# Kernel tuning notes

Measured on AMD Instinct MI355X. Metric: run time of the kernel, lower is better.

Reference implementation:

```python
import jax, jax.numpy as jnp
import numpy as np

E = 8        # num discriminators == num adapters (layer_structure = [1]*8)
D = 1024     # feature_dim
DO = 1024    # out_feature_dim
R = 64       # adapter bottleneck rank
H = 256      # discriminator hidden dim
B, T = 8, 2048


def setup_inputs() -> dict:
    key = jax.random.key(0)
    ks = jax.random.split(key, 12)
    s = lambda k, shape, fan: jax.random.normal(k, shape, jnp.float32) / np.sqrt(fan)
    return {
        "x": jax.random.normal(ks[0], (B, T, D), jnp.float32),
        # base layer (Linear D -> DO)
        "W_base": s(ks[1], (D, DO), D),
        "b_base": jnp.zeros((DO,), jnp.float32),
        # stacked discriminator autoencoders: D -> H -> D
        "Wd1": s(ks[2], (E, D, H), D),
        "bd1": jnp.zeros((E, H), jnp.float32),
        "Wd2": s(ks[3], (E, H, D), H),
        "bd2": jnp.zeros((E, D), jnp.float32),
        # stacked bottleneck adapters: D -> R -> DO
        "Wa_down": s(ks[4], (E, D, R), D),
        "ba_down": jnp.zeros((E, R), jnp.float32),
        "Wa_up": s(ks[5], (E, R, DO), R),
        "ba_up": jnp.zeros((E, DO), jnp.float32),
    }


def reference(x, W_base, b_base, Wd1, bd1, Wd2, bd2, Wa_down, ba_down, Wa_up, ba_up):
    # base path
    base = jnp.einsum("btd,do->bto", x, W_base) + b_base

    # all discriminators in parallel (stack_module_state + vmap equivalent)
    h = jax.nn.relu(jnp.einsum("btd,edh->ebth", x, Wd1) + bd1[:, None, None, :])
    recon = jnp.einsum("ebth,ehd->ebtd", h, Wd2) + bd2[:, None, None, :]
    # per-(discriminator, sample) reconstruction loss -> [E, B]
    losses = jnp.mean((recon - x[None]) ** 2, axis=(2, 3))

    # top-1 routing: argmin over discriminators per sample; identity mapping to adapters
    idx = jnp.argmin(losses, axis=0)  # [B]

    # grouped adapter forward: gather per-sample weights, batched GEMM
    a = jax.nn.relu(jnp.einsum("btd,bdr->btr", x, Wa_down[idx]) + ba_down[idx][:, None, :])
    adapter_out = jnp.einsum("btr,bro->bto", a, Wa_up[idx]) + ba_up[idx][:, None, :]

    return base + adapter_out
```

## Files before the change

kernel.cpp:

```cpp
#include <hip/hip_runtime.h>

typedef __bf16 bf16x8 __attribute__((ext_vector_type(8)));
typedef float f32x4 __attribute__((ext_vector_type(4)));
typedef unsigned short ushort_t;

#define THREADS 256
#define PTHREADS 512

__device__ __forceinline__ unsigned short f2bf(float f) {
  unsigned int u = __builtin_bit_cast(unsigned int, f);
  u += 0x7fffu + ((u >> 16) & 1u);
  return (unsigned short)(u >> 16);
}

__device__ __forceinline__ float bf2f(ushort_t u) {
  unsigned int v = ((unsigned int)u) << 16;
  return __builtin_bit_cast(float, v);
}

__device__ __forceinline__ void gload_lds16(const ushort_t* g, ushort_t* l) {
  __builtin_amdgcn_global_load_lds(
      (const __attribute__((address_space(1))) void*)g,
      (__attribute__((address_space(3))) void*)l, 16, 0, 0);
}

template <int N>
__device__ __forceinline__ void wait_vmcnt() {
  if constexpr (N == 0)
    asm volatile("s_waitcnt vmcnt(0)" ::: "memory");
  else if constexpr (N == 3)
    asm volatile("s_waitcnt vmcnt(3)" ::: "memory");
  else if constexpr (N == 6)
    asm volatile("s_waitcnt vmcnt(6)" ::: "memory");
}

__device__ __forceinline__ void block_barrier() {
  asm volatile("" ::: "memory");
  __builtin_amdgcn_s_barrier();
  asm volatile("" ::: "memory");
}

__device__ __forceinline__ int argmin8(const float* __restrict__ losses,
                                       int sample) {
  float best = losses[sample];
  int bi = 0;
#pragma unroll
  for (int e = 1; e < 8; ++e) {
    float v = losses[e * 8 + sample];
    if (v < best) { best = v; bi = e; }
  }
  return bi;
}

__global__ void transpose_all_kernel(
    const float* __restrict__ Wd1, const float* __restrict__ Wd2,
    const float* __restrict__ Wb, const float* __restrict__ Wad,
    const float* __restrict__ Wau, const float4* __restrict__ x4,
    ushort_t* __restrict__ Wd1T, ushort_t* __restrict__ Wd2T,
    ushort_t* __restrict__ WbT, ushort_t* __restrict__ WadT,
    ushort_t* __restrict__ WauT, ushort4* __restrict__ x_bf4,
    float* __restrict__ losses) {
  __shared__ float t[32][33];
  int b = blockIdx.x;
  int tx = threadIdx.x, ty = threadIdx.y;
  int ft = ty * 32 + tx;
  if (b == 0 && ft < 64) losses[ft] = 0.f;

  if (b >= 6144) {
    int base = (b - 6144) * 2048 + ft;
#pragma unroll
    for (int i = 0; i < 8; ++i) {
      float4 v = x4[base + i * 256];
      ushort4 o;
      o.x = f2bf(v.x); o.y = f2bf(v.y); o.z = f2bf(v.z); o.w = f2bf(v.w);
      x_bf4[base + i * 256] = o;
    }
    return;
  }

  const float* src;
  ushort_t* dst;
  int R, C, z, cx, ry;
  if (b < 2048) {
    src = Wd1; dst = Wd1T; R = 1024; C = 256;
    z = b >> 8; int rem = b & 255; cx = rem & 7; ry = rem >> 3;
  } else if (b < 4096) {
    int bb = b - 2048;
    src = Wd2; dst = Wd2T; R = 256; C = 1024;
    z = bb >> 8; int rem = bb & 255; cx = rem & 31; ry = rem >> 5;
  } else if (b < 5120) {
    int bb = b - 4096;
    src = Wb; dst = WbT; R = 1024; C = 1024;
    z = 0; cx = bb & 31; ry = bb >> 5;
  } else if (b < 5632) {
    int bb = b - 5120;
    src = Wad; dst = WadT; R = 1024; C = 64;
    z = bb >> 6; int rem = bb & 63; cx = rem & 1; ry = rem >> 1;
  } else {
    int bb = b - 5632;
    src = Wau; dst = WauT; R = 64; C = 1024;
    z = bb >> 6; int rem = bb & 63; cx = rem & 31; ry = rem >> 5;
  }
  size_t zoff = (size_t)z * R * C;
  src += zoff; dst += zoff;
  int c0 = cx * 32, r0 = ry * 32;
#pragma unroll
  for (int i = 0; i < 4; ++i)
    t[ty + 8 * i][tx] = src[(size_t)(r0 + ty + 8 * i) * C + c0 + tx];
  __syncthreads();
#pragma unroll
  for (int i = 0; i < 4; ++i)
    dst[(size_t)(c0 + ty + 8 * i) * R + r0 + tx] = f2bf(t[tx][ty + 8 * i]);
}

#define ACC_ZERO(acc, MM, NN)                        \
  _Pragma("unroll") for (int _i = 0; _i < MM; ++_i)  \
  _Pragma("unroll") for (int _j = 0; _j < NN; ++_j)  \
      acc[_i][_j] = (f32x4){0.f, 0.f, 0.f, 0.f};

__device__ __forceinline__ int sw(int row) { return (row >> 1) & 3; }

__device__ __forceinline__ bf16x8 frag_sw(const ushort_t* lds, int row, int q) {
  int slot = q ^ sw(row);
  return *(const bf16x8*)(lds + (row * 4 + slot) * 8);
}

template <int BM, int BN, int NT>
__device__ __forceinline__ void stage_p(const ushort_t* __restrict__ A,
                                        size_t lda, int arow0,
                                        const ushort_t* __restrict__ BT,
                                        size_t ldb, int brow0, int k0,
                                        ushort_t* As, ushort_t* Bs, int tid) {
#pragma unroll
  for (int i = 0; i < BM * 4 / NT; ++i) {
    int c = tid + i * NT;
    int row = c >> 2, slot = c & 3;
    int g = slot ^ sw(row);
    gload_lds16(A + (size_t)(arow0 + row) * lda + k0 + g * 8, As + c * 8);
  }
#pragma unroll
  for (int i = 0; i < BN * 4 / NT; ++i) {
    int c = tid + i * NT;
    int row = c >> 2, slot = c & 3;
    int g = slot ^ sw(row);
    gload_lds16(BT + (size_t)(brow0 + row) * ldb + k0 + g * 8, Bs + c * 8);
  }
}

#define PIPE_LDS_BYTES ((3 * (256 * 32) + 3 * (128 * 32)) * 2)

template <int BM, int BN>
__device__ __forceinline__ void pipe_kloop84(const ushort_t* __restrict__ A,
                                             size_t lda, int arow0,
                                             const ushort_t* __restrict__ BT,
                                             size_t ldb, int brow0, int K,
                                             ushort_t* smem, int tid, int wm,
                                             int wn, f32x4 acc[8][4]) {
  constexpr int ASLOT = BM * 32, BSLOT = BN * 32;
  ushort_t* Asl = smem;
  ushort_t* Bsl = smem + 3 * ASLOT;
  int lane = tid & 63;
  int r = lane & 15, q = lane >> 4;
  int nt = K >> 5;
  stage_p<BM, BN, THREADS>(A, lda, arow0, BT, ldb, brow0, 0, Asl, Bsl, tid);
  if (nt > 1)
    stage_p<BM, BN, THREADS>(A, lda, arow0, BT, ldb, brow0, 32, Asl + ASLOT,
                             Bsl + BSLOT, tid);
  for (int t = 0; t < nt; ++t) {
    if (t + 1 < nt)
      wait_vmcnt<6>();
    else
      wait_vmcnt<0>();
    block_barrier();
    if (t + 2 < nt) {
      int s = (t + 2) % 3;
      stage_p<BM, BN, THREADS>(A, lda, arow0, BT, ldb, brow0, (t + 2) * 32,
                               Asl + s * ASLOT, Bsl + s * BSLOT, tid);
    }
    int cur = t % 3;
    const ushort_t* Ac = Asl + cur * ASLOT;
    const ushort_t* Bc = Bsl + cur * BSLOT;
    bf16x8 af[8], bg[4];
#pragma unroll
    for (int mi = 0; mi < 8; ++mi)
      af[mi] = frag_sw(Ac, wm * 128 + mi * 16 + r, q);
#pragma unroll
    for (int ni = 0; ni < 4; ++ni)
      bg[ni] = frag_sw(Bc, wn * 64 + ni * 16 + r, q);
    __builtin_amdgcn_s_setprio(1);
#pragma unroll
    for (int mi = 0; mi < 8; ++mi)
#pragma unroll
      for (int ni = 0; ni < 4; ++ni)
        acc[mi][ni] = __builtin_amdgcn_mfma_f32_16x16x32_bf16(
            af[mi], bg[ni], acc[mi][ni], 0, 0, 0);
    __builtin_amdgcn_s_setprio(0);
  }
  block_barrier();
}

template <int BM, int BN>
__device__ __forceinline__ void pipe_kloop44(const ushort_t* __restrict__ A,
                                             size_t lda, int arow0,
                                             const ushort_t* __restrict__ BT,
                                             size_t ldb, int brow0, int K,
                                             ushort_t* smem, int tid, int wm,
                                             int wn, f32x4 acc[4][4]) {
  constexpr int ASLOT = BM * 32, BSLOT = BN * 32;
  ushort_t* Asl = smem;
  ushort_t* Bsl = smem + 3 * ASLOT;
  int lane = tid & 63;
  int r = lane & 15, q = lane >> 4;
  int nt = K >> 5;
  stage_p<BM, BN, PTHREADS>(A, lda, arow0, BT, ldb, brow0, 0, Asl, Bsl, tid);
  if (nt > 1)
    stage_p<BM, BN, PTHREADS>(A, lda, arow0, BT, ldb, brow0, 32, Asl + ASLOT,
                              Bsl + BSLOT, tid);
  for (int t = 0; t < nt; ++t) {
    if (t + 1 < nt)
      wait_vmcnt<3>();
    else
      wait_vmcnt<0>();
    block_barrier();
    if (t + 2 < nt) {
      int s = (t + 2) % 3;
      stage_p<BM, BN, PTHREADS>(A, lda, arow0, BT, ldb, brow0, (t + 2) * 32,
                                Asl + s * ASLOT, Bsl + s * BSLOT, tid);
    }
    int cur = t % 3;
    const ushort_t* Ac = Asl + cur * ASLOT;
    const ushort_t* Bc = Bsl + cur * BSLOT;
    bf16x8 af[4], bg[4];
#pragma unroll
    for (int mi = 0; mi < 4; ++mi)
      af[mi] = frag_sw(Ac, wm * 64 + mi * 16 + r, q);
#pragma unroll
    for (int ni = 0; ni < 4; ++ni)
      bg[ni] = frag_sw(Bc, wn * 64 + ni * 16 + r, q);
    __builtin_amdgcn_s_setprio(1);
#pragma unroll
    for (int mi = 0; mi < 4; ++mi)
#pragma unroll
      for (int ni = 0; ni < 4; ++ni)
        acc[mi][ni] = __builtin_amdgcn_mfma_f32_16x16x32_bf16(
            af[mi], bg[ni], acc[mi][ni], 0, 0, 0);
    __builtin_amdgcn_s_setprio(0);
  }
  block_barrier();
}

__global__ __launch_bounds__(THREADS, 2) void disc_h_kernel(
    const ushort_t* __restrict__ x_bf, const ushort_t* __restrict__ Wd1T,
    const float* __restrict__ bd1, ushort_t* __restrict__ h) {
  extern __shared__ ushort_t smem[];
  int b = blockIdx.x;
  int work = (b & 7) * 128 + (b >> 3);
  int m0 = (work >> 4) * 256;
  int n0 = (work & 15) * 128;
  int tid = threadIdx.x, wid = tid >> 6, lane = tid & 63;
  int wm = wid >> 1, wn = wid & 1;
  f32x4 acc[8][4];
  ACC_ZERO(acc, 8, 4);
  pipe_kloop84<256, 128>(x_bf, 1024, m0, Wd1T, 1024, n0, 1024, smem, tid, wm,
                         wn, acc);
  int r = lane & 15, q = lane >> 4;
#pragma unroll
  for (int ni = 0; ni < 4; ++ni) {
    int col = n0 + wn * 64 + ni * 16 + r;
    float bias = bd1[col];
    int e = col >> 8, nn = col & 255;
    ushort_t* hp = h + (size_t)e * 16384 * 256 + nn;
#pragma unroll
    for (int mi = 0; mi < 8; ++mi) {
      int rowb = m0 + wm * 128 + mi * 16 + q * 4;
#pragma unroll
      for (int j = 0; j < 4; ++j) {
        float v = fmaxf(acc[mi][ni][j] + bias, 0.f);
        hp[(size_t)(rowb + j) * 256] = f2bf(v);
      }
    }
  }
}

__global__ __launch_bounds__(PTHREADS, 4) void disc_loss_kernel(
    const ushort_t* __restrict__ h, const ushort_t* __restrict__ Wd2T,
    const float* __restrict__ bd2, const ushort_t* __restrict__ x_bf,
    float* __restrict__ losses) {
  extern __shared__ ushort_t smem[];
  __shared__ float red[8];
  int b = blockIdx.x;
  int work = (b & 7) * 512 + (b >> 3);
  int e = work >> 9;
  int m0 = ((work >> 3) & 63) * 256;
  int n0 = (work & 7) * 128;
  int tid = threadIdx.x, wid = tid >> 6, lane = tid & 63;
  int wm = wid >> 1, wn = wid & 1;
  int r = lane & 15, q = lane >> 4;
  const ushort_t* hA = h + (size_t)e * 16384 * 256;
  const ushort_t* W2 = Wd2T + (size_t)e * 1024 * 256;

  f32x4 acc[4][4];
  ACC_ZERO(acc, 4, 4);
  pipe_kloop44<256, 128>(hA, 256, m0, W2, 256, n0, 256, smem, tid, wm, wn,
                         acc);

  float s = 0.f;
#pragma unroll
  for (int ni = 0; ni < 4; ++ni) {
    int colg = n0 + wn * 64 + ni * 16 + r;
    float bias = bd2[e * 1024 + colg];
#pragma unroll
    for (int mi = 0; mi < 4; ++mi) {
      int rowg = m0 + wm * 64 + mi * 16 + q * 4;
#pragma unroll
      for (int j = 0; j < 4; ++j) {
        float v = acc[mi][ni][j] + bias -
                  bf2f(x_bf[(size_t)(rowg + j) * 1024 + colg]);
        s += v * v;
      }
    }
  }
#pragma unroll
  for (int off = 32; off > 0; off >>= 1) s += __shfl_down(s, off);
  if (lane == 0) red[wid] = s;
  __syncthreads();
  if (tid == 0) {
    float t = 0.f;
#pragma unroll
    for (int i = 0; i < 8; ++i) t += red[i];
    atomicAdd(&losses[e * 8 + (m0 >> 11)], t);
  }
}

__global__ __launch_bounds__(THREADS, 2) void final_kernel(
    const ushort_t* __restrict__ x, const ushort_t* __restrict__ WbT,
    const float* __restrict__ b_base, const ushort_t* __restrict__ a,
    const ushort_t* __restrict__ WauT, const float* __restrict__ ba_up,
    const float* __restrict__ losses, float* __restrict__ out) {
  extern __shared__ ushort_t smem[];
  int b = blockIdx.x;
  int work = (b & 7) * 64 + (b >> 3);
  int m0 = (work >> 3) * 256;
  int n0 = (work & 7) * 128;
  int e = argmin8(losses, m0 >> 11);
  int tid = threadIdx.x, wid = tid >> 6, lane = tid & 63;
  int wm = wid >> 1, wn = wid & 1;
  f32x4 acc[8][4];
  ACC_ZERO(acc, 8, 4);
  pipe_kloop84<256, 128>(x, 1024, m0, WbT, 1024, n0, 1024, smem, tid, wm, wn,
                         acc);
  pipe_kloop84<256, 128>(a, 64, m0, WauT + (size_t)e * 1024 * 64, 64, n0, 64,
                         smem, tid, wm, wn, acc);
  int r = lane & 15, q = lane >> 4;
#pragma unroll
  for (int ni = 0; ni < 4; ++ni) {
    int col = n0 + wn * 64 + ni * 16 + r;
    float bias = b_base[col] + ba_up[e * 1024 + col];
#pragma unroll
    for (int mi = 0; mi < 8; ++mi) {
      int rowb = m0 + wm * 128 + mi * 16 + q * 4;
#pragma unroll
      for (int j = 0; j < 4; ++j)
        out[(size_t)(rowb + j) * 1024 + col] = acc[mi][ni][j] + bias;
    }
  }
}

__global__ __launch_bounds__(THREADS) void adapter_down_kernel(
    const ushort_t* __restrict__ x, const ushort_t* __restrict__ WadT,
    const float* __restrict__ ba_down, const float* __restrict__ losses,
    ushort_t* __restrict__ a) {
  __shared__ ushort_t As[64 * 32], Bs[64 * 32];
  int m0 = blockIdx.x * 64;
  int e = argmin8(losses, m0 >> 11);
  int tid = threadIdx.x, wid = tid >> 6, lane = tid & 63;
  int r = lane & 15, q = lane >> 4;
  const ushort_t* W = WadT + (size_t)e * 64 * 1024;
  f32x4 acc[4];
#pragma unroll
  for (int ni = 0; ni < 4; ++ni) acc[ni] = (f32x4){0.f, 0.f, 0.f, 0.f};
  for (int k0 = 0; k0 < 1024; k0 += 32) {
#pragma unroll
    for (int p = 0; p < 2; ++p) {
      int c = tid + p * THREADS;
      int row = c >> 2, slot = c & 3;
      int g = slot ^ sw(row);
      if (c < 256)
        gload_lds16(x + (size_t)(m0 + row) * 1024 + k0 + g * 8, As + c * 8);
      else
        gload_lds16(W + (size_t)(row - 64) * 1024 + k0 + g * 8,
                    Bs + (c - 256) * 8);
    }
    __syncthreads();
    bf16x8 af = frag_sw(As, wid * 16 + r, q);
#pragma unroll
    for (int ni = 0; ni < 4; ++ni) {
      bf16x8 bg = frag_sw(Bs, ni * 16 + r, q);
      acc[ni] = __builtin_amdgcn_mfma_f32_16x16x32_bf16(af, bg, acc[ni], 0, 0, 0);
    }
    __syncthreads();
  }
#pragma unroll
  for (int ni = 0; ni < 4; ++ni) {
    int col = ni * 16 + r;
    float bias = ba_down[e * 64 + col];
    int rowb = m0 + wid * 16 + q * 4;
#pragma unroll
    for (int j = 0; j < 4; ++j) {
      float v = fmaxf(acc[ni][j] + bias, 0.f);
      a[(size_t)(rowb + j) * 64 + col] = f2bf(v);
    }
  }
}

extern "C" void kernel_launch(void* const* d_in, const int* in_sizes, int n_in,
                              void* d_out, int out_size, void* d_ws,
                              size_t ws_size, hipStream_t stream) {
  const float* x       = (const float*)d_in[0];
  const float* W_base  = (const float*)d_in[1];
  const float* b_base  = (const float*)d_in[2];
  const float* Wd1     = (const float*)d_in[3];
  const float* bd1     = (const float*)d_in[4];
  const float* Wd2     = (const float*)d_in[5];
  const float* bd2     = (const float*)d_in[6];
  const float* Wa_down = (const float*)d_in[7];
  const float* ba_down = (const float*)d_in[8];
  const float* Wa_up   = (const float*)d_in[9];
  const float* ba_up   = (const float*)d_in[10];
  float* out = (float*)d_out;

  char* w = (char*)d_ws;
  size_t off = 0;
  auto alloc = [&](size_t bytes) {
    void* p = w + off;
    off += (bytes + 255) & ~(size_t)255;
    return p;
  };
  ushort_t* x_bf = (ushort_t*)alloc((size_t)16384 * 1024 * 2);
  ushort_t* Wd1T = (ushort_t*)alloc((size_t)8 * 256 * 1024 * 2);
  ushort_t* Wd2T = (ushort_t*)alloc((size_t)8 * 1024 * 256 * 2);
  ushort_t* WbT  = (ushort_t*)alloc((size_t)1024 * 1024 * 2);
  ushort_t* WadT = (ushort_t*)alloc((size_t)8 * 64 * 1024 * 2);
  ushort_t* WauT = (ushort_t*)alloc((size_t)8 * 1024 * 64 * 2);
  ushort_t* abuf = (ushort_t*)alloc((size_t)16384 * 64 * 2);
  float* losses  = (float*)alloc(64 * 4);
  size_t hbytes = (size_t)8 * 16384 * 256 * 2;
  ushort_t* h = (ws_size >= off + hbytes) ? (ushort_t*)alloc(hbytes)
                                          : (ushort_t*)d_out;

  (void)hipFuncSetAttribute((const void*)disc_h_kernel,
                            hipFuncAttributeMaxDynamicSharedMemorySize,
                            PIPE_LDS_BYTES);
  (void)hipFuncSetAttribute((const void*)disc_loss_kernel,
                            hipFuncAttributeMaxDynamicSharedMemorySize,
                            PIPE_LDS_BYTES);
  (void)hipFuncSetAttribute((const void*)final_kernel,
                            hipFuncAttributeMaxDynamicSharedMemorySize,
                            PIPE_LDS_BYTES);

  transpose_all_kernel<<<8192, dim3(32, 8), 0, stream>>>(
      Wd1, Wd2, W_base, Wa_down, Wa_up, (const float4*)x, Wd1T, Wd2T, WbT,
      WadT, WauT, (ushort4*)x_bf, losses);

  disc_h_kernel<<<1024, THREADS, PIPE_LDS_BYTES, stream>>>(x_bf, Wd1T, bd1, h);
  disc_loss_kernel<<<4096, PTHREADS, PIPE_LDS_BYTES, stream>>>(h, Wd2T, bd2,
                                                               x_bf, losses);

  adapter_down_kernel<<<256, THREADS, 0, stream>>>(x_bf, WadT, ba_down,
                                                   losses, abuf);
  final_kernel<<<512, THREADS, PIPE_LDS_BYTES, stream>>>(x_bf, WbT, b_base,
                                                         abuf, WauT, ba_up,
                                                         losses, out);
}
```

Measured before the change: 264.5 us.

## Process two N-tiles per disc_loss block with a continuous staging pipeline

Each disc_loss block now covers a 256x256 output tile as two consecutive 128-column sub-tiles, running one 16-step software pipeline that prefetches the second sub-tile's operands while the first sub-tile's epilogue (bias, x reload, squared error) runs. The grid is halved to 2048 blocks. This removes per-block pipeline ramp-up and drain and halves the atomic reductions, and it lets the epilogue overlap with loads. In exchange it holds a second accumulator set, which raises register pressure and could lower occupancy, and there are fewer, longer blocks.

```diff
diff --git a/kernel.cpp b/kernel.cpp
--- a/kernel.cpp
+++ b/kernel.cpp
@@ -199,56 +199,6 @@
   block_barrier();
 }
 
-template <int BM, int BN>
-__device__ __forceinline__ void pipe_kloop44(const ushort_t* __restrict__ A,
-                                             size_t lda, int arow0,
-                                             const ushort_t* __restrict__ BT,
-                                             size_t ldb, int brow0, int K,
-                                             ushort_t* smem, int tid, int wm,
-                                             int wn, f32x4 acc[4][4]) {
-  constexpr int ASLOT = BM * 32, BSLOT = BN * 32;
-  ushort_t* Asl = smem;
-  ushort_t* Bsl = smem + 3 * ASLOT;
-  int lane = tid & 63;
-  int r = lane & 15, q = lane >> 4;
-  int nt = K >> 5;
-  stage_p<BM, BN, PTHREADS>(A, lda, arow0, BT, ldb, brow0, 0, Asl, Bsl, tid);
-  if (nt > 1)
-    stage_p<BM, BN, PTHREADS>(A, lda, arow0, BT, ldb, brow0, 32, Asl + ASLOT,
-                              Bsl + BSLOT, tid);
-  for (int t = 0; t < nt; ++t) {
-    if (t + 1 < nt)
-      wait_vmcnt<3>();
-    else
-      wait_vmcnt<0>();
-    block_barrier();
-    if (t + 2 < nt) {
-      int s = (t + 2) % 3;
-      stage_p<BM, BN, PTHREADS>(A, lda, arow0, BT, ldb, brow0, (t + 2) * 32,
-                                Asl + s * ASLOT, Bsl + s * BSLOT, tid);
-    }
-    int cur = t % 3;
-    const ushort_t* Ac = Asl + cur * ASLOT;
-    const ushort_t* Bc = Bsl + cur * BSLOT;
-    bf16x8 af[4], bg[4];
-#pragma unroll
-    for (int mi = 0; mi < 4; ++mi)
-      af[mi] = frag_sw(Ac, wm * 64 + mi * 16 + r, q);
-#pragma unroll
-    for (int ni = 0; ni < 4; ++ni)
-      bg[ni] = frag_sw(Bc, wn * 64 + ni * 16 + r, q);
-    __builtin_amdgcn_s_setprio(1);
-#pragma unroll
-    for (int mi = 0; mi < 4; ++mi)
-#pragma unroll
-      for (int ni = 0; ni < 4; ++ni)
-        acc[mi][ni] = __builtin_amdgcn_mfma_f32_16x16x32_bf16(
-            af[mi], bg[ni], acc[mi][ni], 0, 0, 0);
-    __builtin_amdgcn_s_setprio(0);
-  }
-  block_barrier();
-}
-
 __global__ __launch_bounds__(THREADS, 2) void disc_h_kernel(
     const ushort_t* __restrict__ x_bf, const ushort_t* __restrict__ Wd1T,
     const float* __restrict__ bd1, ushort_t* __restrict__ h) {
@@ -288,23 +238,57 @@
     float* __restrict__ losses) {
   extern __shared__ ushort_t smem[];
   __shared__ float red[8];
+  constexpr int ASLOT = 256 * 32, BSLOT = 128 * 32;
+  ushort_t* Asl = smem;
+  ushort_t* Bsl = smem + 3 * ASLOT;
+
   int b = blockIdx.x;
-  int work = (b & 7) * 512 + (b >> 3);
-  int e = work >> 9;
-  int m0 = ((work >> 3) & 63) * 256;
-  int n0 = (work & 7) * 128;
+  int work = (b & 7) * 256 + (b >> 3);
+  int e = work >> 8;
+  int m0 = ((work >> 2) & 63) * 256;
+  int n0 = (work & 3) * 256;
   int tid = threadIdx.x, wid = tid >> 6, lane = tid & 63;
   int wm = wid >> 1, wn = wid & 1;
   int r = lane & 15, q = lane >> 4;
   const ushort_t* hA = h + (size_t)e * 16384 * 256;
   const ushort_t* W2 = Wd2T + (size_t)e * 1024 * 256;
 
-  f32x4 acc[4][4];
-  ACC_ZERO(acc, 4, 4);
-  pipe_kloop44<256, 128>(hA, 256, m0, W2, 256, n0, 256, smem, tid, wm, wn,
-                         acc);
-
-  float s = 0.f;
+  auto stage_s = [&](int s) {
+    int u = s >> 3, k0 = (s & 7) * 32, slot = s % 3;
+    stage_p<256, 128, PTHREADS>(hA, 256, m0, W2, 256, n0 + u * 128, k0,
+                                Asl + slot * ASLOT, Bsl + slot * BSLOT, tid);
+  };
+
+  float loss = 0.f;
+  f32x4 accA[4][4], accB[4][4];
+  ACC_ZERO(accA, 4, 4);
+  ACC_ZERO(accB, 4, 4);
+
+  stage_s(0);
+  stage_s(1);
+  for (int t = 0; t < 8; ++t) {
+    wait_vmcnt<3>();
+    block_barrier();
+    stage_s(t + 2);
+    int cur = t % 3;
+    const ushort_t* Ac = Asl + cur * ASLOT;
+    const ushort_t* Bc = Bsl + cur * BSLOT;
+    bf16x8 af[4], bg[4];
+#pragma unroll
+    for (int mi = 0; mi < 4; ++mi)
+      af[mi] = frag_sw(Ac, wm * 64 + mi * 16 + r, q);
+#pragma unroll
+    for (int ni = 0; ni < 4; ++ni)
+      bg[ni] = frag_sw(Bc, wn * 64 + ni * 16 + r, q);
+    __builtin_amdgcn_s_setprio(1);
+#pragma unroll
+    for (int mi = 0; mi < 4; ++mi)
+#pragma unroll
+      for (int ni = 0; ni < 4; ++ni)
+        accA[mi][ni] = __builtin_amdgcn_mfma_f32_16x16x32_bf16(
+            af[mi], bg[ni], accA[mi][ni], 0, 0, 0);
+    __builtin_amdgcn_s_setprio(0);
+  }
 #pragma unroll
   for (int ni = 0; ni < 4; ++ni) {
     int colg = n0 + wn * 64 + ni * 16 + r;
@@ -314,15 +298,57 @@
       int rowg = m0 + wm * 64 + mi * 16 + q * 4;
 #pragma unroll
       for (int j = 0; j < 4; ++j) {
-        float v = acc[mi][ni][j] + bias -
+        float v = accA[mi][ni][j] + bias -
                   bf2f(x_bf[(size_t)(rowg + j) * 1024 + colg]);
-        s += v * v;
+        loss += v * v;
       }
     }
   }
-#pragma unroll
-  for (int off = 32; off > 0; off >>= 1) s += __shfl_down(s, off);
-  if (lane == 0) red[wid] = s;
+  for (int t = 8; t < 16; ++t) {
+    if (t + 1 < 16)
+      wait_vmcnt<3>();
+    else
+      wait_vmcnt<0>();
+    block_barrier();
+    if (t + 2 < 16) stage_s(t + 2);
+    int cur = t % 3;
+    const ushort_t* Ac = Asl + cur * ASLOT;
+    const ushort_t* Bc = Bsl + cur * BSLOT;
+    bf16x8 af[4], bg[4];
+#pragma unroll
+    for (int mi = 0; mi < 4; ++mi)
+      af[mi] = frag_sw(Ac, wm * 64 + mi * 16 + r, q);
+#pragma unroll
+    for (int ni = 0; ni < 4; ++ni)
+      bg[ni] = frag_sw(Bc, wn * 64 + ni * 16 + r, q);
+    __builtin_amdgcn_s_setprio(1);
+#pragma unroll
+    for (int mi = 0; mi < 4; ++mi)
+#pragma unroll
+      for (int ni = 0; ni < 4; ++ni)
+        accB[mi][ni] = __builtin_amdgcn_mfma_f32_16x16x32_bf16(
+            af[mi], bg[ni], accB[mi][ni], 0, 0, 0);
+    __builtin_amdgcn_s_setprio(0);
+  }
+#pragma unroll
+  for (int ni = 0; ni < 4; ++ni) {
+    int colg = n0 + 128 + wn * 64 + ni * 16 + r;
+    float bias = bd2[e * 1024 + colg];
+#pragma unroll
+    for (int mi = 0; mi < 4; ++mi) {
+      int rowg = m0 + wm * 64 + mi * 16 + q * 4;
+#pragma unroll
+      for (int j = 0; j < 4; ++j) {
+        float v = accB[mi][ni][j] + bias -
+                  bf2f(x_bf[(size_t)(rowg + j) * 1024 + colg]);
+        loss += v * v;
+      }
+    }
+  }
+
+#pragma unroll
+  for (int off = 32; off > 0; off >>= 1) loss += __shfl_down(loss, off);
+  if (lane == 0) red[wid] = loss;
   __syncthreads();
   if (tid == 0) {
     float t = 0.f;
@@ -463,7 +489,7 @@
       WadT, WauT, (ushort4*)x_bf, losses);
 
   disc_h_kernel<<<1024, THREADS, PIPE_LDS_BYTES, stream>>>(x_bf, Wd1T, bd1, h);
-  disc_loss_kernel<<<4096, PTHREADS, PIPE_LDS_BYTES, stream>>>(h, Wd2T, bd2,
+  disc_loss_kernel<<<2048, PTHREADS, PIPE_LDS_BYTES, stream>>>(h, Wd2T, bd2,
                                                                x_bf, losses);
 
   adapter_down_kernel<<<256, THREADS, 0, stream>>>(x_bf, WadT, ba_down,
```

Result: slower. 375.7 us, median of 2 (+42.1%).
